# Performance work log

Hardware: AMD Instinct MI355X
Metric: run time of the kernel (lower is better)

## Reference

```python
import jax, jax.numpy as jnp
import numpy as np

OUT_H = OUT_W = 7
SAMPLE = 2          # sample_num (sampling_ratio)
SCALE = 0.125       # spatial_scale
IMG = 1600.0        # image size implied by scale * feature size


def setup_inputs() -> dict:
    key = jax.random.key(0)
    k1, k2, k3, k4 = jax.random.split(key, 4)
    N, C, H, W = 2, 256, 200, 200
    K = 1000
    features = jax.random.normal(k1, (N, C, H, W), dtype=jnp.float32)
    b = jax.random.randint(k2, (K,), 0, N).astype(jnp.float32)
    xy = jax.random.uniform(k3, (K, 4), dtype=jnp.float32) * IMG  # raw corners
    x1 = jnp.minimum(xy[:, 0], xy[:, 2]); x2 = jnp.maximum(xy[:, 0], xy[:, 2])
    y1 = jnp.minimum(xy[:, 1], xy[:, 3]); y2 = jnp.maximum(xy[:, 1], xy[:, 3])
    rois = jnp.stack([b, x1, y1, x2, y2], axis=1)  # [K,5]
    return {"features": features, "rois": rois}


def _roi_align(features, rois):
    # Faithful port of torchvision roi_align (aligned=False, sampling_ratio=SAMPLE)
    N, C, H, W = features.shape
    K = rois.shape[0]
    b = rois[:, 0].astype(jnp.int32)
    x1 = rois[:, 1] * SCALE; y1 = rois[:, 2] * SCALE
    x2 = rois[:, 3] * SCALE; y2 = rois[:, 4] * SCALE
    roi_w = jnp.maximum(x2 - x1, 1.0)  # aligned=False forces min size 1
    roi_h = jnp.maximum(y2 - y1, 1.0)
    bin_w = roi_w / OUT_W
    bin_h = roi_h / OUT_H

    # sample coordinates: [K, out*S] along each axis
    pbin = jnp.repeat(jnp.arange(OUT_H, dtype=jnp.float32), SAMPLE)      # bin index
    sub = jnp.tile(jnp.arange(SAMPLE, dtype=jnp.float32) + 0.5, OUT_H)   # sub-sample offset
    ys = y1[:, None] + pbin[None] * bin_h[:, None] + sub[None] * bin_h[:, None] / SAMPLE  # [K,Ny]
    xs = x1[:, None] + pbin[None] * bin_w[:, None] + sub[None] * bin_w[:, None] / SAMPLE  # [K,Nx]

    def axis_terms(c, size):
        valid = (c >= -1.0) & (c <= size)        # torch: zero outside [-1, size]
        c = jnp.maximum(c, 0.0)
        lo0 = jnp.floor(c).astype(jnp.int32)
        hi_edge = lo0 >= size - 1
        lo = jnp.where(hi_edge, size - 1, lo0)
        hi = jnp.where(hi_edge, size - 1, lo0 + 1)
        c = jnp.where(hi_edge, jnp.float32(size - 1), c)
        l = c - lo.astype(jnp.float32)           # fractional part
        return valid, lo, hi, l

    vy, yl, yh, ly = axis_terms(ys, H)
    vx, xl, xh, lx = axis_terms(xs, W)
    hy, hx = 1.0 - ly, 1.0 - lx

    def gather(yi, xi):
        # [K,Ny,Nx,C] gather with per-roi batch index
        return features[b[:, None, None], :, yi[:, :, None], xi[:, None, :]]

    val = (hy[:, :, None] * hx[:, None, :])[..., None] * gather(yl, xl) \
        + (hy[:, :, None] * lx[:, None, :])[..., None] * gather(yl, xh) \
        + (ly[:, :, None] * hx[:, None, :])[..., None] * gather(yh, xl) \
        + (ly[:, :, None] * lx[:, None, :])[..., None] * gather(yh, xh)
    mask = (vy[:, :, None] & vx[:, None, :])[..., None]
    val = jnp.where(mask, val, 0.0)

    # average SAMPLE x SAMPLE points per bin -> [K,C,OUT_H,OUT_W]
    val = val.reshape(K, OUT_H, SAMPLE, OUT_W, SAMPLE, C).mean(axis=(2, 4))
    return val.transpose(0, 3, 1, 2)


def reference(features, rois):
    return _roi_align(features, rois)
```

## Files before the change

kernel.cpp:

```cpp
#include <hip/hip_runtime.h>

constexpr int C = 256, H = 200, W = 200, NB = 2;
constexpr int PH = 7, PW = 7;
constexpr int NS = 14;
constexpr float SCALE = 0.125f;
constexpr int CG = 32, NCG = C / CG;
constexpr int CGF = 8, NGROUPF = C / CGF;

typedef float    f32x4 __attribute__((ext_vector_type(4)));
typedef _Float16 h2    __attribute__((ext_vector_type(2)));

__global__ __launch_bounds__(256) void transpose_kernel(
    const float* __restrict__ feat, ushort* __restrict__ T)
{
    __shared__ float tile[W][36];
    int B = blockIdx.x;
    int y = B % H;
    int s = B / H;
    int nb = s & 1, cg = s >> 1;

    int t = threadIdx.x;
    {
        int cl  = t >> 3;
        int xi4 = t & 7;
        const float* src = feat + (((size_t)nb * C + cg * CG + cl) * H + y) * W;
        for (int s4 = xi4; s4 < W / 4; s4 += 8) {
            float4 v = *reinterpret_cast<const float4*>(src + 4 * s4);
            int x = 4 * s4;
            tile[x + 0][cl] = v.x; tile[x + 1][cl] = v.y;
            tile[x + 2][cl] = v.z; tile[x + 3][cl] = v.w;
        }
    }
    __syncthreads();
    {
        int c4 = (t & 7) * 4;
        ushort* dstrow = T + (((size_t)s * H + y) * W) * CG;
        for (int px = t >> 3; px < W; px += 32) {
            float4 v = *reinterpret_cast<const float4*>(&tile[px][c4]);
            uint2 o;
            o.x = __builtin_bit_cast(uint, __builtin_amdgcn_cvt_pkrtz(v.x, v.y));
            o.y = __builtin_bit_cast(uint, __builtin_amdgcn_cvt_pkrtz(v.z, v.w));
            *reinterpret_cast<uint2*>(dstrow + px * CG + c4) = o;
        }
    }
}

__global__ __launch_bounds__(256) void gather_kernel(
    const ushort* __restrict__ T, const float* __restrict__ rois,
    float* __restrict__ out, int K)
{
    __shared__ float s_out[CG * 49];

    int B  = blockIdx.x;
    int cg = B & 7;
    int j  = B >> 3;
    int p  = j / K, k = j - p * K;

    const float* r = rois + (size_t)k * 5;
    int b = (int)r[0];
    if (b != p) return;

    int t = threadIdx.x;
    if (t < 49 * 4) {
        int bin = t >> 2, q = t & 3;
        int ph = bin / 7, pw = bin - ph * 7;

        float x1 = r[1]*SCALE, y1 = r[2]*SCALE, x2 = r[3]*SCALE, y2 = r[4]*SCALE;
        float bw = fmaxf(x2 - x1, 1.0f) * (1.0f / PW);
        float bh = fmaxf(y2 - y1, 1.0f) * (1.0f / PH);

        int   yr[2][2]; float wy[2][2];
        int   xr[2][2]; float wx[2][2];
        #pragma unroll
        for (int s = 0; s < 2; ++s) {
            float y = y1 + (float)ph * bh + ((float)s + 0.5f) * bh * 0.5f;
            bool v = (y >= -1.0f) && (y <= (float)H);
            float yc = fmaxf(y, 0.0f);
            int lo = (int)yc, hi;
            if (lo >= H - 1) { lo = H - 1; hi = H - 1; yc = (float)(H - 1); }
            else             { hi = lo + 1; }
            float l = yc - (float)lo;
            yr[s][0] = lo; yr[s][1] = hi;
            wy[s][0] = v ? 1.0f - l : 0.0f;
            wy[s][1] = v ? l        : 0.0f;
        }
        #pragma unroll
        for (int s = 0; s < 2; ++s) {
            float x = x1 + (float)pw * bw + ((float)s + 0.5f) * bw * 0.5f;
            bool v = (x >= -1.0f) && (x <= (float)W);
            float xc = fmaxf(x, 0.0f);
            int lo = (int)xc, hi;
            if (lo >= W - 1) { lo = W - 1; hi = W - 1; xc = (float)(W - 1); }
            else             { hi = lo + 1; }
            float l = xc - (float)lo;
            xr[s][0] = lo; xr[s][1] = hi;
            wx[s][0] = v ? 1.0f - l : 0.0f;
            wx[s][1] = v ? l        : 0.0f;
        }

        int  offv[16];
        uint wgtv[16];
        #pragma unroll
        for (int cr = 0; cr < 16; ++cr) {
            int sy = (cr >> 3) & 1, sx = (cr >> 2) & 1, cy = (cr >> 1) & 1, cx = cr & 1;
            offv[cr] = (yr[sy][cy] * W + xr[sx][cx]) * CG;
            float w = wy[sy][cy] * wx[sx][cx] * 0.25f;
            wgtv[cr] = __builtin_bit_cast(uint, __builtin_amdgcn_cvt_pkrtz(w, w));
        }

        const ushort* slab = T + ((size_t)(cg * NB + p) * H * W) * CG + q * 8;
        uint4 d[16];
        #pragma unroll
        for (int cr = 0; cr < 16; ++cr)
            d[cr] = *reinterpret_cast<const uint4*>(slab + offv[cr]);

        h2 a01 = {0, 0}, a23 = {0, 0}, a45 = {0, 0}, a67 = {0, 0};
        #define H2(u) (__builtin_bit_cast(h2, (uint)(u)))
        #pragma unroll
        for (int cr = 0; cr < 16; ++cr) {
            h2 wpk = H2(wgtv[cr]);
            a01 += H2(d[cr].x) * wpk;  a23 += H2(d[cr].y) * wpk;
            a45 += H2(d[cr].z) * wpk;  a67 += H2(d[cr].w) * wpk;
        }
        #undef H2

        float* so = s_out + (8 * q) * 49 + bin;
        so[0*49] = (float)a01.x; so[1*49] = (float)a01.y;
        so[2*49] = (float)a23.x; so[3*49] = (float)a23.y;
        so[4*49] = (float)a45.x; so[5*49] = (float)a45.y;
        so[6*49] = (float)a67.x; so[7*49] = (float)a67.y;
    }
    __syncthreads();

    float* oslab = out + ((size_t)k * C + cg * CG) * (PH * PW);
    for (int i4 = t; i4 < (CG * 49) / 4; i4 += 256) {
        f32x4 v = *reinterpret_cast<const f32x4*>(s_out + 4 * i4);
        __builtin_nontemporal_store(v, reinterpret_cast<f32x4*>(oslab + 4 * i4));
    }
}

struct __attribute__((packed, aligned(4))) f2 { float a, b; };

__global__ __launch_bounds__(256) void roi_align_fallback(
    const float* __restrict__ feat, const float* __restrict__ rois,
    float* __restrict__ out, int K)
{
    __shared__ int   s_ylo[NS], s_yhi[NS];
    __shared__ float s_wy[NS][2];
    __shared__ int   s_xb[NS];
    __shared__ float s_wx[NS][2];

    int B   = blockIdx.x;
    int xcd = B & 7;
    int j   = B >> 3;
    int p   = j / K, k = j - p * K;
    int cb  = (p * 8 + xcd) * CGF;

    const float* r = rois + (size_t)k * 5;
    int   b  = (int)r[0];
    float x1 = r[1]*SCALE, y1 = r[2]*SCALE, x2 = r[3]*SCALE, y2 = r[4]*SCALE;
    float bw = fmaxf(x2 - x1, 1.0f) * (1.0f / PW);
    float bh = fmaxf(y2 - y1, 1.0f) * (1.0f / PH);

    int t = threadIdx.x;
    if (t < NS) {
        int ph = t >> 1, s = t & 1;
        float y = y1 + (float)ph * bh + ((float)s + 0.5f) * bh * 0.5f;
        bool v = (y >= -1.0f) && (y <= (float)H);
        float yc = fmaxf(y, 0.0f);
        int lo = (int)yc, hi;
        if (lo >= H - 1) { lo = H - 1; hi = H - 1; yc = (float)(H - 1); }
        else             { hi = lo + 1; }
        float l = yc - (float)lo;
        s_ylo[t] = lo; s_yhi[t] = hi;
        s_wy[t][0] = v ? 1.0f - l : 0.0f;
        s_wy[t][1] = v ? l        : 0.0f;
    } else if (t >= 64 && t < 64 + NS) {
        int i = t - 64, pw = i >> 1, s = i & 1;
        float x = x1 + (float)pw * bw + ((float)s + 0.5f) * bw * 0.5f;
        bool v = (x >= -1.0f) && (x <= (float)W);
        float xc = fmaxf(x, 0.0f);
        int lo = (int)xc;
        if (lo >= W - 1) {
            s_xb[i] = W - 2; s_wx[i][0] = 0.0f; s_wx[i][1] = v ? 1.0f : 0.0f;
        } else {
            float l = xc - (float)lo;
            s_xb[i] = lo; s_wx[i][0] = v ? 1.0f - l : 0.0f; s_wx[i][1] = v ? l : 0.0f;
        }
    }
    __syncthreads();

    const float* img = feat + (size_t)b * (C * H * W);
    float* out_base = out + ((size_t)k * C + cb) * (PH * PW);

    for (int i = t; i < CGF * PH * PW; i += 256) {
        int cl  = i / (PH * PW);
        int bin = i - cl * (PH * PW);
        int ph  = bin / PW;
        int pw  = bin - ph * PW;
        const float* plane = img + (size_t)(cb + cl) * (H * W);

        float acc = 0.0f;
        #pragma unroll
        for (int sy = 0; sy < 2; ++sy) {
            int ysi = 2 * ph + sy;
            const float* rlo = plane + s_ylo[ysi] * W;
            const float* rhi = plane + s_yhi[ysi] * W;
            float hy = s_wy[ysi][0], ly = s_wy[ysi][1];
            #pragma unroll
            for (int sx = 0; sx < 2; ++sx) {
                int xsi = 2 * pw + sx;
                int xb = s_xb[xsi];
                float w0 = s_wx[xsi][0], w1 = s_wx[xsi][1];
                f2 vlo = *reinterpret_cast<const f2*>(rlo + xb);
                f2 vhi = *reinterpret_cast<const f2*>(rhi + xb);
                acc += hy * (w0 * vlo.a + w1 * vlo.b)
                     + ly * (w0 * vhi.a + w1 * vhi.b);
            }
        }
        __builtin_nontemporal_store(acc * 0.25f, &out_base[i]);
    }
}

extern "C" void kernel_launch(void* const* d_in, const int* in_sizes, int n_in,
                              void* d_out, int out_size, void* d_ws, size_t ws_size,
                              hipStream_t stream) {
    const float* feat = (const float*)d_in[0];
    const float* rois = (const float*)d_in[1];
    float* out = (float*)d_out;
    int K = in_sizes[1] / 5;

    size_t need = (size_t)NCG * NB * H * W * CG * sizeof(ushort);
    if (ws_size >= need) {
        ushort* T = (ushort*)d_ws;
        int tblocks = NCG * NB * H;
        transpose_kernel<<<tblocks, 256, 0, stream>>>(feat, T);
        gather_kernel<<<K * NCG * NB, 256, 0, stream>>>(T, rois, out, K);
    } else {
        roi_align_fallback<<<K * NGROUPF, 256, 0, stream>>>(feat, rois, out, K);
    }
}
```

Before: 51.58 us.

## Process two ROIs per gather block, prefetching the second during the first's stores

The gather kernel now handles a pair of consecutive ROIs per block, so the grid is half as large. After the first ROI's results are in shared memory, the block issues the 16 corner loads for the second ROI before writing the first ROI's output, so load latency overlaps the stores. The corner-table computation moves into a shared helper. In exchange, each thread holds an extra 16 uint4 prefetch registers, which lowers occupancy. Pairs where only one ROI belongs to the block's batch still occupy a whole block.

```diff
diff --git a/kernel.cpp b/kernel.cpp
--- a/kernel.cpp
+++ b/kernel.cpp
@@ -45,85 +45,91 @@
     }
 }
 
+__device__ __forceinline__ void corner_tables(
+    const float* __restrict__ r, int ph, int pw, int* offv, uint* wgtv)
+{
+    float x1 = r[1]*SCALE, y1 = r[2]*SCALE, x2 = r[3]*SCALE, y2 = r[4]*SCALE;
+    float bw = fmaxf(x2 - x1, 1.0f) * (1.0f / PW);
+    float bh = fmaxf(y2 - y1, 1.0f) * (1.0f / PH);
+
+    int yr[2][2]; float wy[2][2];
+    int xr[2][2]; float wx[2][2];
+    #pragma unroll
+    for (int s = 0; s < 2; ++s) {
+        float y = y1 + (float)ph * bh + ((float)s + 0.5f) * bh * 0.5f;
+        bool v = (y >= -1.0f) && (y <= (float)H);
+        float yc = fmaxf(y, 0.0f);
+        int lo = (int)yc, hi;
+        if (lo >= H - 1) { lo = H - 1; hi = H - 1; yc = (float)(H - 1); }
+        else             { hi = lo + 1; }
+        float l = yc - (float)lo;
+        yr[s][0] = lo; yr[s][1] = hi;
+        wy[s][0] = v ? 1.0f - l : 0.0f;
+        wy[s][1] = v ? l        : 0.0f;
+    }
+    #pragma unroll
+    for (int s = 0; s < 2; ++s) {
+        float x = x1 + (float)pw * bw + ((float)s + 0.5f) * bw * 0.5f;
+        bool v = (x >= -1.0f) && (x <= (float)W);
+        float xc = fmaxf(x, 0.0f);
+        int lo = (int)xc, hi;
+        if (lo >= W - 1) { lo = W - 1; hi = W - 1; xc = (float)(W - 1); }
+        else             { hi = lo + 1; }
+        float l = xc - (float)lo;
+        xr[s][0] = lo; xr[s][1] = hi;
+        wx[s][0] = v ? 1.0f - l : 0.0f;
+        wx[s][1] = v ? l        : 0.0f;
+    }
+    #pragma unroll
+    for (int cr = 0; cr < 16; ++cr) {
+        int sy = (cr >> 3) & 1, sx = (cr >> 2) & 1, cy = (cr >> 1) & 1, cx = cr & 1;
+        offv[cr] = (yr[sy][cy] * W + xr[sx][cx]) * CG;
+        float w = wy[sy][cy] * wx[sx][cx] * 0.25f;
+        wgtv[cr] = __builtin_bit_cast(uint, __builtin_amdgcn_cvt_pkrtz(w, w));
+    }
+}
+
+#define H2C(u) (__builtin_bit_cast(h2, (uint)(u)))
+
 __global__ __launch_bounds__(256) void gather_kernel(
     const ushort* __restrict__ T, const float* __restrict__ rois,
-    float* __restrict__ out, int K)
+    float* __restrict__ out, int K, int PK)
 {
     __shared__ float s_out[CG * 49];
 
     int B  = blockIdx.x;
     int cg = B & 7;
     int j  = B >> 3;
-    int p  = j / K, k = j - p * K;
-
-    const float* r = rois + (size_t)k * 5;
-    int b = (int)r[0];
-    if (b != p) return;
+    int p  = j / PK, jj = j - p * PK;
+    int k0 = 2 * jj, k1 = k0 + 1;
+
+    const float* r0 = rois + (size_t)k0 * 5;
+    bool have1 = (k1 < K);
+    const float* r1 = rois + (size_t)(have1 ? k1 : k0) * 5;
+    bool do0 = ((int)r0[0] == p);
+    bool do1 = have1 && ((int)r1[0] == p);
+    if (!do0 && !do1) return;
 
     int t = threadIdx.x;
-    if (t < 49 * 4) {
-        int bin = t >> 2, q = t & 3;
-        int ph = bin / 7, pw = bin - ph * 7;
-
-        float x1 = r[1]*SCALE, y1 = r[2]*SCALE, x2 = r[3]*SCALE, y2 = r[4]*SCALE;
-        float bw = fmaxf(x2 - x1, 1.0f) * (1.0f / PW);
-        float bh = fmaxf(y2 - y1, 1.0f) * (1.0f / PH);
-
-        int   yr[2][2]; float wy[2][2];
-        int   xr[2][2]; float wx[2][2];
-        #pragma unroll
-        for (int s = 0; s < 2; ++s) {
-            float y = y1 + (float)ph * bh + ((float)s + 0.5f) * bh * 0.5f;
-            bool v = (y >= -1.0f) && (y <= (float)H);
-            float yc = fmaxf(y, 0.0f);
-            int lo = (int)yc, hi;
-            if (lo >= H - 1) { lo = H - 1; hi = H - 1; yc = (float)(H - 1); }
-            else             { hi = lo + 1; }
-            float l = yc - (float)lo;
-            yr[s][0] = lo; yr[s][1] = hi;
-            wy[s][0] = v ? 1.0f - l : 0.0f;
-            wy[s][1] = v ? l        : 0.0f;
-        }
-        #pragma unroll
-        for (int s = 0; s < 2; ++s) {
-            float x = x1 + (float)pw * bw + ((float)s + 0.5f) * bw * 0.5f;
-            bool v = (x >= -1.0f) && (x <= (float)W);
-            float xc = fmaxf(x, 0.0f);
-            int lo = (int)xc, hi;
-            if (lo >= W - 1) { lo = W - 1; hi = W - 1; xc = (float)(W - 1); }
-            else             { hi = lo + 1; }
-            float l = xc - (float)lo;
-            xr[s][0] = lo; xr[s][1] = hi;
-            wx[s][0] = v ? 1.0f - l : 0.0f;
-            wx[s][1] = v ? l        : 0.0f;
-        }
-
-        int  offv[16];
-        uint wgtv[16];
-        #pragma unroll
-        for (int cr = 0; cr < 16; ++cr) {
-            int sy = (cr >> 3) & 1, sx = (cr >> 2) & 1, cy = (cr >> 1) & 1, cx = cr & 1;
-            offv[cr] = (yr[sy][cy] * W + xr[sx][cx]) * CG;
-            float w = wy[sy][cy] * wx[sx][cx] * 0.25f;
-            wgtv[cr] = __builtin_bit_cast(uint, __builtin_amdgcn_cvt_pkrtz(w, w));
-        }
-
-        const ushort* slab = T + ((size_t)(cg * NB + p) * H * W) * CG + q * 8;
+    int bin = t >> 2, q = t & 3;
+    int ph = bin / 7, pw = bin - ph * 7;
+    bool lane_ok = (t < 49 * 4);
+    const ushort* slab = T + ((size_t)(cg * NB + p) * H * W) * CG + q * 8;
+
+    if (lane_ok && do0) {
+        int  offv[16]; uint wgtv[16];
+        corner_tables(r0, ph, pw, offv, wgtv);
         uint4 d[16];
         #pragma unroll
         for (int cr = 0; cr < 16; ++cr)
             d[cr] = *reinterpret_cast<const uint4*>(slab + offv[cr]);
-
-        h2 a01 = {0, 0}, a23 = {0, 0}, a45 = {0, 0}, a67 = {0, 0};
-        #define H2(u) (__builtin_bit_cast(h2, (uint)(u)))
+        h2 a01 = {0,0}, a23 = {0,0}, a45 = {0,0}, a67 = {0,0};
         #pragma unroll
         for (int cr = 0; cr < 16; ++cr) {
-            h2 wpk = H2(wgtv[cr]);
-            a01 += H2(d[cr].x) * wpk;  a23 += H2(d[cr].y) * wpk;
-            a45 += H2(d[cr].z) * wpk;  a67 += H2(d[cr].w) * wpk;
-        }
-        #undef H2
-
+            h2 wpk = H2C(wgtv[cr]);
+            a01 += H2C(d[cr].x) * wpk;  a23 += H2C(d[cr].y) * wpk;
+            a45 += H2C(d[cr].z) * wpk;  a67 += H2C(d[cr].w) * wpk;
+        }
         float* so = s_out + (8 * q) * 49 + bin;
         so[0*49] = (float)a01.x; so[1*49] = (float)a01.y;
         so[2*49] = (float)a23.x; so[3*49] = (float)a23.y;
@@ -132,12 +138,51 @@
     }
     __syncthreads();
 
-    float* oslab = out + ((size_t)k * C + cg * CG) * (PH * PW);
-    for (int i4 = t; i4 < (CG * 49) / 4; i4 += 256) {
-        f32x4 v = *reinterpret_cast<const f32x4*>(s_out + 4 * i4);
-        __builtin_nontemporal_store(v, reinterpret_cast<f32x4*>(oslab + 4 * i4));
-    }
-}
+    uint4 e[16];
+    uint  wgt1[16];
+    if (lane_ok && do1) {
+        int offv1[16];
+        corner_tables(r1, ph, pw, offv1, wgt1);
+        #pragma unroll
+        for (int cr = 0; cr < 16; ++cr)
+            e[cr] = *reinterpret_cast<const uint4*>(slab + offv1[cr]);
+    }
+
+    if (do0) {
+        float* oslab = out + ((size_t)k0 * C + cg * CG) * (PH * PW);
+        for (int i4 = t; i4 < (CG * 49) / 4; i4 += 256) {
+            f32x4 v = *reinterpret_cast<const f32x4*>(s_out + 4 * i4);
+            __builtin_nontemporal_store(v, reinterpret_cast<f32x4*>(oslab + 4 * i4));
+        }
+    }
+    if (!do1) return;
+
+    __syncthreads();
+    if (lane_ok) {
+        h2 a01 = {0,0}, a23 = {0,0}, a45 = {0,0}, a67 = {0,0};
+        #pragma unroll
+        for (int cr = 0; cr < 16; ++cr) {
+            h2 wpk = H2C(wgt1[cr]);
+            a01 += H2C(e[cr].x) * wpk;  a23 += H2C(e[cr].y) * wpk;
+            a45 += H2C(e[cr].z) * wpk;  a67 += H2C(e[cr].w) * wpk;
+        }
+        float* so = s_out + (8 * q) * 49 + bin;
+        so[0*49] = (float)a01.x; so[1*49] = (float)a01.y;
+        so[2*49] = (float)a23.x; so[3*49] = (float)a23.y;
+        so[4*49] = (float)a45.x; so[5*49] = (float)a45.y;
+        so[6*49] = (float)a67.x; so[7*49] = (float)a67.y;
+    }
+    __syncthreads();
+
+    {
+        float* oslab = out + ((size_t)k1 * C + cg * CG) * (PH * PW);
+        for (int i4 = t; i4 < (CG * 49) / 4; i4 += 256) {
+            f32x4 v = *reinterpret_cast<const f32x4*>(s_out + 4 * i4);
+            __builtin_nontemporal_store(v, reinterpret_cast<f32x4*>(oslab + 4 * i4));
+        }
+    }
+}
+#undef H2C
 
 struct __attribute__((packed, aligned(4))) f2 { float a, b; };
 
@@ -235,7 +280,8 @@
         ushort* T = (ushort*)d_ws;
         int tblocks = NCG * NB * H;
         transpose_kernel<<<tblocks, 256, 0, stream>>>(feat, T);
-        gather_kernel<<<K * NCG * NB, 256, 0, stream>>>(T, rois, out, K);
+        int PK = (K + 1) / 2;
+        gather_kernel<<<PK * NB * 8, 256, 0, stream>>>(T, rois, out, K, PK);
     } else {
         roi_align_fallback<<<K * NGROUPF, 256, 0, stream>>>(feat, rois, out, K);
     }
```

Result: slower. 54.44 us (+5.5%).
